# Kernel optimization log

Measured on AMD Instinct MI355X. Metric: run time of the kernel, lower is better.

The kernel has to match this reference:

```python
import jax, jax.numpy as jnp
import numpy as np

D_IN = 512
D_OUT = 512
NUM_HEADS = 8
HEAD_DIM = D_OUT // NUM_HEADS


def setup_inputs() -> dict:
    key = jax.random.key(0)
    ks = jax.random.split(key, 6)
    b, t, n = 4, 32, 256
    scale = 1.0 / np.sqrt(D_IN)
    return {
        "x": jax.random.normal(ks[0], (b, t, n, D_IN), dtype=jnp.float32),
        "Wq": jax.random.normal(ks[1], (D_IN, D_OUT), dtype=jnp.float32) * scale,
        "Wk": jax.random.normal(ks[2], (D_IN, D_OUT), dtype=jnp.float32) * scale,
        "Wv": jax.random.normal(ks[3], (D_IN, D_OUT), dtype=jnp.float32) * scale,
        "Wo": jax.random.normal(ks[4], (D_OUT, D_OUT), dtype=jnp.float32) * scale,
        "bo": jax.random.normal(ks[5], (D_OUT,), dtype=jnp.float32) * 0.01,
    }


def reference(x, Wq, Wk, Wv, Wo, bo):
    b, t, n, _ = x.shape
    h, hd = NUM_HEADS, HEAD_DIM
    # QKV projections (no bias, qkv_bias=False)
    q = (x @ Wq).reshape(b, t, n, h, hd)
    k = (x @ Wk).reshape(b, t, n, h, hd)
    v = (x @ Wv).reshape(b, t, n, h, hd)
    # attention over tokens, per (batch, timestamp, head)
    scores = jnp.einsum('btqhd,btkhd->bthqk', q, k) / np.sqrt(hd).astype(jnp.float32)
    weights = jax.nn.softmax(scores, axis=-1)
    # dropout p=0.0 (eval / deterministic reference) -> identity
    ctx = jnp.einsum('bthqk,btkhd->btqhd', weights, v).reshape(b, t, n, D_OUT)
    return ctx @ Wo + bo
```

## Files before the change

kernel.cpp:

```cpp
#include <hip/hip_runtime.h>
#include <hip/hip_bf16.h>

typedef __attribute__((ext_vector_type(8))) short bf16x8;
typedef __attribute__((ext_vector_type(4))) float f32x4;

#define MFMA_16x16x32(a,b,c) __builtin_amdgcn_mfma_f32_16x16x32_bf16((a),(b),(c),0,0,0)

__device__ __forceinline__ unsigned short f2bf(float f){
  unsigned int u = __float_as_uint(f);
  u += 0x7FFFu + ((u >> 16) & 1u);
  return (unsigned short)(u >> 16);
}

__device__ __forceinline__ unsigned int cvtpk_bf16(float lo, float hi){
  unsigned int r;
  asm("v_cvt_pk_bf16_f32 %0, %1, %2" : "=v"(r) : "v"(lo), "v"(hi));
  return r;
}

__device__ __forceinline__ void async16(const void* g, void* l){
  __builtin_amdgcn_global_load_lds((const __attribute__((address_space(1))) void*)g,
                                   (__attribute__((address_space(3))) void*)l,
                                   16, 0, 0);
}

#define FENCE asm volatile("" ::: "memory")
#define BARRL do{ asm volatile("s_waitcnt lgkmcnt(0)" ::: "memory"); \
                  __builtin_amdgcn_s_barrier(); FENCE; }while(0)

__global__ __launch_bounds__(256) void prep_weights(const float* __restrict__ Wq,
                                                    const float* __restrict__ Wk,
                                                    const float* __restrict__ Wv,
                                                    const float* __restrict__ Wo,
                                                    unsigned short* __restrict__ WqkvT,
                                                    unsigned short* __restrict__ WoT){
  int idx = blockIdx.x*256 + threadIdx.x;
  int stride = gridDim.x*256;
  const int T1 = 1536*512;
  const int total = T1 + 512*512;
  for (int o = idx; o < total; o += stride){
    if (o < T1){
      int n = o >> 9, k = o & 511;
      const float* W = (n < 512) ? Wq : ((n < 1024) ? Wk : Wv);
      WqkvT[o] = f2bf(W[k*512 + (n & 511)]);
    } else {
      int o2 = o - T1;
      int n = o2 >> 9, k = o2 & 511;
      WoT[o2] = f2bf(Wo[k*512 + n]);
    }
  }
}

template<bool AFP32, bool BIAS, bool OUTBF16>
__global__ __launch_bounds__(512, 2) void gemm4(const void* __restrict__ Av,
                                                const unsigned short* __restrict__ Bt,
                                                float* __restrict__ Cf, unsigned short* __restrict__ Cb,
                                                const float* __restrict__ bias,
                                                int K, int NB, int ldc){
  __shared__ __attribute__((aligned(16))) char ldsA[2][16384];
  __shared__ __attribute__((aligned(16))) char ldsB[2][16384];
  const int tid = threadIdx.x;
  const int lane = tid & 63, w = tid >> 6;
  const int wr = w >> 1, wc = w & 1;
  const int l15 = lane & 15, lhi = lane >> 4;

  const int cpx = gridDim.x >> 3;
  const int bid = (blockIdx.x & 7) * cpx + (blockIdx.x >> 3);
  const int bm = bid / NB, bn = bid % NB;

  const int row0 = tid >> 3;
  const int srcb = ((tid & 7) << 4) ^ ((row0 & 7) << 4);
  const size_t rK2 = (size_t)K * 2;
  const unsigned short* A16 = (const unsigned short*)Av;
  const float*          A32 = (const float*)Av;
  const char* Ab = (const char*)(A16 + (size_t)(bm*128 + row0) * K) + srcb;
  const char* Bb = (const char*)(Bt  + (size_t)(bn*128 + row0) * K) + srcb;

  const int arow = (w << 4) + (lhi << 2);
  const int au = l15;
  const float* xbase = A32 + (size_t)(bm*128 + arow) * K + au*4;

#define STG_A16(p,kt) do{ _Pragma("unroll") for (int j=0;j<2;++j) \
    async16(Ab + (size_t)(j*64)*rK2 + (size_t)(kt)*2, ldsA[p] + j*8192 + w*1024); }while(0)
#define STG_B(p,kt) do{ _Pragma("unroll") for (int j=0;j<2;++j) \
    async16(Bb + (size_t)(j*64)*rK2 + (size_t)(kt)*2, ldsB[p] + j*8192 + w*1024); }while(0)

#define LDA_G(dst, kt) do{ _Pragma("unroll") for (int j=0;j<4;++j) \
    dst[j] = *reinterpret_cast<const float4*>(xbase + (size_t)j*K + (kt)); }while(0)
#define WRA(p, src) do{ _Pragma("unroll") for (int j=0;j<4;++j){ \
    const int r_ = arow + j; \
    char* pw_ = ldsA[p] + r_*128 + ((((au>>1) ^ (r_&7))<<4) + ((au&1)<<3)); \
    uint2 v_; v_.x = cvtpk_bf16(src[j].x, src[j].y); \
              v_.y = cvtpk_bf16(src[j].z, src[j].w); \
    *reinterpret_cast<uint2*>(pw_) = v_; } }while(0)

#define LDAF(p) do{ _Pragma("unroll") for (int f=0;f<2;++f){ \
    const int m_ = wr*32 + f*16 + l15; \
    const char* base_ = ldsA[p] + m_*128; \
    af[f][0] = *reinterpret_cast<const bf16x8*>(base_ + (((lhi<<4))      ^ ((m_&7)<<4))); \
    af[f][1] = *reinterpret_cast<const bf16x8*>(base_ + ((64 + (lhi<<4)) ^ ((m_&7)<<4))); } }while(0)
#define LDBF(dst, p, nh) do{ _Pragma("unroll") for (int n2=0;n2<2;++n2){ \
    const int n_ = wc*64 + ((nh)*2+n2)*16 + l15; \
    const char* base_ = ldsB[p] + n_*128; \
    dst[n2][0] = *reinterpret_cast<const bf16x8*>(base_ + (((lhi<<4))      ^ ((n_&7)<<4))); \
    dst[n2][1] = *reinterpret_cast<const bf16x8*>(base_ + ((64 + (lhi<<4)) ^ ((n_&7)<<4))); } }while(0)
#define MFQ(nh, B_) do{ _Pragma("unroll") for (int f=0;f<2;++f) \
    _Pragma("unroll") for (int n2=0;n2<2;++n2) \
    _Pragma("unroll") for (int kk=0;kk<2;++kk) \
      acc[f][(nh)*2+n2] = MFMA_16x16x32(af[f][kk], B_[n2][kk], acc[f][(nh)*2+n2]); }while(0)

  f32x4 acc[2][4];
  const f32x4 fzero = {0.f,0.f,0.f,0.f};
  #pragma unroll
  for (int i=0;i<2;++i)
    #pragma unroll
    for (int j=0;j<4;++j) acc[i][j] = fzero;
  bf16x8 af[2][2], bf0[2][2], bfc[2][2];
  float4 areg[4];
  const int nt = K >> 6;

  if constexpr (AFP32){
    float4 a0[4], a1[4];
    LDA_G(a0, 0); LDA_G(a1, 64);
    STG_B(0, 0); STG_B(1, 64);
    asm volatile("s_waitcnt vmcnt(8)" ::: "memory");
    WRA(0, a0);
    asm volatile("s_waitcnt vmcnt(2)" ::: "memory");
    WRA(1, a1);
    if (nt > 2) LDA_G(areg, 128);
    asm volatile("s_waitcnt lgkmcnt(0)" ::: "memory");
    __builtin_amdgcn_s_barrier(); FENCE;
  } else {
    STG_A16(0,0); STG_B(0,0); STG_A16(1,64); STG_B(1,64);
    asm volatile("s_waitcnt vmcnt(4)" ::: "memory");
    __builtin_amdgcn_s_barrier(); FENCE;
  }

  for (int t = 0; t < nt; ++t){
    const int p = t & 1;
    const int kt2 = (t+2) << 6, kt3 = (t+3) << 6;
    LDAF(p); LDBF(bf0, p, 0); LDBF(bfc, p, 1);
    __builtin_amdgcn_s_setprio(1); MFQ(0, bf0); __builtin_amdgcn_s_setprio(0);
    BARRL;
    if constexpr (AFP32){
      asm volatile("s_waitcnt vmcnt(0)" ::: "memory");
      if (t+2 < nt){ WRA(p, areg); STG_B(p, kt2); }
      if (t+3 < nt) LDA_G(areg, kt3);
      __builtin_amdgcn_s_setprio(1); MFQ(1, bfc); __builtin_amdgcn_s_setprio(0);
      if (t+1 < nt) BARRL;
    } else {
      if (t+2 < nt){ STG_A16(p, kt2); STG_B(p, kt2); }
      __builtin_amdgcn_s_setprio(1); MFQ(1, bfc); __builtin_amdgcn_s_setprio(0);
      if (t+1 < nt){
        if (t+2 < nt) asm volatile("s_waitcnt vmcnt(4) lgkmcnt(0)" ::: "memory");
        else          asm volatile("s_waitcnt vmcnt(0) lgkmcnt(0)" ::: "memory");
        __builtin_amdgcn_s_barrier(); FENCE;
      }
    }
  }

  #pragma unroll
  for (int mi=0;mi<2;++mi){
    const int r = bm*128 + wr*32 + mi*16 + lhi*4;
    #pragma unroll
    for (int ni=0;ni<4;++ni){
      const int cc = bn*128 + wc*64 + ni*16 + l15;
      float bv = 0.f;
      if (BIAS) bv = bias[cc];
      #pragma unroll
      for (int i=0;i<4;++i){
        float v = acc[mi][ni][i] + bv;
        if (OUTBF16) Cb[(size_t)(r+i)*ldc + cc] = f2bf(v);
        else         Cf[(size_t)(r+i)*ldc + cc] = v;
      }
    }
  }
#undef STG_A16
#undef STG_B
#undef LDA_G
#undef WRA
#undef LDAF
#undef LDBF
#undef MFQ
}

__global__ __launch_bounds__(256) void attn_kernel(const unsigned short* __restrict__ qkv,
                                                   unsigned short* __restrict__ ctx){
  __shared__ __attribute__((aligned(16))) unsigned short Ks[256*64];
  __shared__ __attribute__((aligned(16))) unsigned short Vst[64*264];

  const int bid = blockIdx.x;
  const int h = bid & 7, bt = bid >> 3;
  const int r0 = bt << 8;
  const int tid = threadIdx.x;
  const int lane = tid & 63, w = tid >> 6;
  const int l15 = lane & 15, lhi = lane >> 4;
  const char* qkvB = (const char*)qkv;
  const f32x4 fzero = {0.f,0.f,0.f,0.f};

  bf16x8 qf[4][2];
  #pragma unroll
  for (int st=0; st<4; ++st){
    int q0 = w*64 + st*16;
    #pragma unroll
    for (int kk=0; kk<2; ++kk)
      qf[st][kk] = *reinterpret_cast<const bf16x8*>(
          qkvB + ((size_t)(r0 + q0 + l15)*1536 + h*64 + kk*32 + lhi*8)*2);
  }

  #pragma unroll
  for (int j=0;j<8;++j){
    int c = (w*8+j)*64 + lane;
    int tok = c >> 3;
    int src = ((c & 7) << 4) ^ ((tok & 7) << 4);
    async16(qkvB + ((size_t)(r0 + tok)*1536 + 512 + h*64)*2 + src,
            (char*)Ks + ((w*8+j) << 10));
  }
  {
    const char* vbase = qkvB + ((size_t)(r0 + tid)*1536 + 1024 + h*64)*2;
    #pragma unroll
    for (int j=0;j<8;++j){
      bf16x8 vv = *reinterpret_cast<const bf16x8*>(vbase + (j<<4));
      #pragma unroll
      for (int e=0;e<8;++e)
        Vst[(j*8+e)*264 + tid] = (unsigned short)vv[e];
    }
  }
  __syncthreads();

  const int ga2 = (lhi & 1) << 1;
  const int lA = l15 + (ga2 << 4);
  const int lB = lA + 16;
  const bool odd = (lhi >> 1) != 0;

  #pragma unroll
  for (int st=0; st<4; ++st){
    const int q0 = w*64 + st*16;

    f32x4 S[16];
    #pragma unroll
    for (int t=0;t<16;++t) S[t] = fzero;
    #pragma unroll
    for (int kk=0;kk<2;++kk){
      #pragma unroll
      for (int t=0;t<16;++t){
        int tok = t*16 + l15;
        int off = tok*128 + (((kk<<6) + (lhi<<4)) ^ ((tok & 7) << 4));
        bf16x8 kf = *reinterpret_cast<const bf16x8*>((const char*)Ks + off);
        S[t] = MFMA_16x16x32(kf, qf[st][kk], S[t]);
      }
    }

    float m = S[0][0];
    #pragma unroll
    for (int t=0;t<16;++t)
      #pragma unroll
      for (int i=0;i<4;++i) m = fmaxf(m, S[t][i]);
    m = fmaxf(m, __shfl_xor(m, 16));
    m = fmaxf(m, __shfl_xor(m, 32));

    float l = 0.f;
    unsigned int P2[32];
    #pragma unroll
    for (int t=0;t<16;++t){
      float p0 = __expf((S[t][0] - m) * 0.125f);
      float p1 = __expf((S[t][1] - m) * 0.125f);
      float p2 = __expf((S[t][2] - m) * 0.125f);
      float p3 = __expf((S[t][3] - m) * 0.125f);
      l += (p0 + p1) + (p2 + p3);
      P2[2*t]   = cvtpk_bf16(p0, p1);
      P2[2*t+1] = cvtpk_bf16(p2, p3);
    }
    l += __shfl_xor(l, 16);
    l += __shfl_xor(l, 32);
    float rl = 1.0f / l;

    f32x4 O[4];
    #pragma unroll
    for (int dt=0;dt<4;++dt) O[dt] = fzero;
    #pragma unroll
    for (int s=0;s<8;++s){
      unsigned int a0e = __shfl((int)P2[4*s+0], lA), a0o = __shfl((int)P2[4*s+2], lA);
      unsigned int a1e = __shfl((int)P2[4*s+1], lA), a1o = __shfl((int)P2[4*s+3], lA);
      unsigned int b0e = __shfl((int)P2[4*s+0], lB), b0o = __shfl((int)P2[4*s+2], lB);
      unsigned int b1e = __shfl((int)P2[4*s+1], lB), b1o = __shfl((int)P2[4*s+3], lB);
      unsigned int u0 = odd ? a0o : a0e;
      unsigned int u1 = odd ? a1o : a1e;
      unsigned int u2 = odd ? b0o : b0e;
      unsigned int u3 = odd ? b1o : b1e;
      bf16x8 pa;
      reinterpret_cast<unsigned int*>(&pa)[0] = u0;
      reinterpret_cast<unsigned int*>(&pa)[1] = u1;
      reinterpret_cast<unsigned int*>(&pa)[2] = u2;
      reinterpret_cast<unsigned int*>(&pa)[3] = u3;
      #pragma unroll
      for (int dt=0;dt<4;++dt){
        bf16x8 vb = *reinterpret_cast<const bf16x8*>(&Vst[(dt*16 + l15)*264 + s*32 + 8*lhi]);
        O[dt] = MFMA_16x16x32(pa, vb, O[dt]);
      }
    }

    float rl4[4];
    #pragma unroll
    for (int i=0;i<4;++i) rl4[i] = __shfl(rl, lhi*4 + i);
    #pragma unroll
    for (int dt=0;dt<4;++dt){
      int col = h*64 + dt*16 + l15;
      #pragma unroll
      for (int i=0;i<4;++i){
        int row = r0 + q0 + lhi*4 + i;
        ctx[(size_t)row*512 + col] = f2bf(O[dt][i] * rl4[i]);
      }
    }
  }
}

extern "C" void kernel_launch(void* const* d_in, const int* in_sizes, int n_in,
                              void* d_out, int out_size, void* d_ws, size_t ws_size,
                              hipStream_t stream) {
  const float* x  = (const float*)d_in[0];
  const float* Wq = (const float*)d_in[1];
  const float* Wk = (const float*)d_in[2];
  const float* Wv = (const float*)d_in[3];
  const float* Wo = (const float*)d_in[4];
  const float* bo = (const float*)d_in[5];
  float* out = (float*)d_out;

  char* ws = (char*)d_ws;
  unsigned short* ctx   = (unsigned short*)ws;
  unsigned short* qkv   = (unsigned short*)(ws + 33554432);
  unsigned short* WqkvT = (unsigned short*)(ws + 134217728);
  unsigned short* WoT   = (unsigned short*)(ws + 135790592);

  prep_weights<<<512, 256, 0, stream>>>(Wq, Wk, Wv, Wo, WqkvT, WoT);
  gemm4<true, false, true><<<3072, 512, 0, stream>>>(x, WqkvT, nullptr, qkv, nullptr,
                                                     512, 12, 1536);
  attn_kernel<<<1024, 256, 0, stream>>>(qkv, ctx);
  gemm4<false, true, false><<<1024, 512, 0, stream>>>(ctx, WoT, out, nullptr, bo,
                                                      512, 4, 512);
}
```

Measured before the change: 172.7 us.

## Deepen fp32 A-operand prefetch to two register buffers with unrolled K loop

The fp32-A GEMM path now keeps two register staging buffers, so global loads of A run two K-tiles ahead instead of one. The K loop is unrolled by two so each half owns a fixed LDS slot and register buffer, and the waitcnt thresholds are adjusted so the loop no longer drains vmcnt to zero every iteration. This aims to hide global load latency behind MFMA work. In exchange it costs more VGPRs, which may lower occupancy, and it assumes nt is even.

```diff
diff --git a/kernel.cpp b/kernel.cpp
--- a/kernel.cpp
+++ b/kernel.cpp
@@ -116,18 +116,16 @@
     #pragma unroll
     for (int j=0;j<4;++j) acc[i][j] = fzero;
   bf16x8 af[2][2], bf0[2][2], bfc[2][2];
-  float4 areg[4];
+  float4 aregA[4], aregB[4];
   const int nt = K >> 6;
 
   if constexpr (AFP32){
     float4 a0[4], a1[4];
-    LDA_G(a0, 0); LDA_G(a1, 64);
-    STG_B(0, 0); STG_B(1, 64);
+    STG_B(0, 0); STG_B(1, 64); FENCE;
+    LDA_G(a0, 0); LDA_G(a1, 64); FENCE;
+    LDA_G(aregA, 128); LDA_G(aregB, 192); FENCE;
     asm volatile("s_waitcnt vmcnt(8)" ::: "memory");
-    WRA(0, a0);
-    asm volatile("s_waitcnt vmcnt(2)" ::: "memory");
-    WRA(1, a1);
-    if (nt > 2) LDA_G(areg, 128);
+    WRA(0, a0); WRA(1, a1);
     asm volatile("s_waitcnt lgkmcnt(0)" ::: "memory");
     __builtin_amdgcn_s_barrier(); FENCE;
   } else {
@@ -136,27 +134,37 @@
     __builtin_amdgcn_s_barrier(); FENCE;
   }
 
-  for (int t = 0; t < nt; ++t){
-    const int p = t & 1;
-    const int kt2 = (t+2) << 6, kt3 = (t+3) << 6;
-    LDAF(p); LDBF(bf0, p, 0); LDBF(bfc, p, 1);
-    __builtin_amdgcn_s_setprio(1); MFQ(0, bf0); __builtin_amdgcn_s_setprio(0);
-    BARRL;
-    if constexpr (AFP32){
-      asm volatile("s_waitcnt vmcnt(0)" ::: "memory");
-      if (t+2 < nt){ WRA(p, areg); STG_B(p, kt2); }
-      if (t+3 < nt) LDA_G(areg, kt3);
-      __builtin_amdgcn_s_setprio(1); MFQ(1, bfc); __builtin_amdgcn_s_setprio(0);
-      if (t+1 < nt) BARRL;
-    } else {
-      if (t+2 < nt){ STG_A16(p, kt2); STG_B(p, kt2); }
-      __builtin_amdgcn_s_setprio(1); MFQ(1, bfc); __builtin_amdgcn_s_setprio(0);
-      if (t+1 < nt){
-        if (t+2 < nt) asm volatile("s_waitcnt vmcnt(4) lgkmcnt(0)" ::: "memory");
-        else          asm volatile("s_waitcnt vmcnt(0) lgkmcnt(0)" ::: "memory");
-        __builtin_amdgcn_s_barrier(); FENCE;
-      }
-    }
+#define BODY(t_, p_, cur_) do{ \
+    LDAF(p_); LDBF(bf0, p_, 0); LDBF(bfc, p_, 1); \
+    __builtin_amdgcn_s_setprio(1); MFQ(0, bf0); __builtin_amdgcn_s_setprio(0); \
+    BARRL;  \
+    if constexpr (AFP32){ \
+      if ((t_)+2 < nt){ \
+        if ((t_)+3 < nt) asm volatile("s_waitcnt vmcnt(4)" ::: "memory"); \
+        else             asm volatile("s_waitcnt vmcnt(2)" ::: "memory"); \
+        WRA(p_, cur_); FENCE; \
+        STG_B(p_, ((t_)+2) << 6); FENCE; \
+      } \
+      if ((t_)+4 < nt){ LDA_G(cur_, ((t_)+4) << 6); FENCE; } \
+    } else { \
+      if ((t_)+2 < nt){ STG_A16(p_, ((t_)+2) << 6); STG_B(p_, ((t_)+2) << 6); } \
+    } \
+    __builtin_amdgcn_s_setprio(1); MFQ(1, bfc); __builtin_amdgcn_s_setprio(0); \
+    if ((t_)+1 < nt){ \
+      if constexpr (AFP32){ \
+        if ((t_)+3 < nt) asm volatile("s_waitcnt lgkmcnt(0)" ::: "memory"); \
+        else             asm volatile("s_waitcnt vmcnt(0) lgkmcnt(0)" ::: "memory"); \
+      } else { \
+        if ((t_)+2 < nt) asm volatile("s_waitcnt vmcnt(4) lgkmcnt(0)" ::: "memory"); \
+        else             asm volatile("s_waitcnt vmcnt(0) lgkmcnt(0)" ::: "memory"); \
+      } \
+      __builtin_amdgcn_s_barrier(); FENCE; \
+    } \
+  }while(0)
+
+  for (int tt = 0; tt < nt; tt += 2){
+    BODY(tt,   0, aregA);
+    BODY(tt+1, 1, aregB);
   }
 
   #pragma unroll
@@ -175,6 +183,7 @@
       }
     }
   }
+#undef BODY
 #undef STG_A16
 #undef STG_B
 #undef LDA_G
```

New measurement: 202.0 us. 16.9% more time.
